# Performance work log

Measured on AMD Instinct MI355X. Metric: run time of the kernel, lower is better.

The kernel has to match this reference:

```python
import jax, jax.numpy as jnp
import numpy as np

HIDDEN = 2304
N_HEADS = 8
N_KV = 4
HEAD_DIM = 256
WINDOW = 1024
SOFTCAP = 50.0
EPS = 1e-6
SCALING = HEAD_DIM ** -0.5  # (head_dim * query_pre_attn_scalar=1.0) ** -0.5


def _rotate_half(x):
    d = x.shape[-1] // 2
    return jnp.concatenate([-x[..., d:], x[..., :d]], axis=-1)


def setup_inputs() -> dict:
    key = jax.random.key(0)
    ks = jax.random.split(key, 8)
    B, S = 2, 2048
    hidden_states = jax.random.normal(ks[0], (B, S, HIDDEN), dtype=jnp.float32)
    # RoPE tables, theta=10000
    inv_freq = 1.0 / (10000.0 ** (jnp.arange(0, HEAD_DIM, 2, dtype=jnp.float32) / HEAD_DIM))
    pos = jnp.arange(S, dtype=jnp.float32)
    freqs = pos[:, None] * inv_freq[None, :]              # [S, D/2]
    emb = jnp.concatenate([freqs, freqs], axis=-1)        # [S, D]
    cos = jnp.broadcast_to(jnp.cos(emb)[None], (B, S, HEAD_DIM)).astype(jnp.float32)
    sin = jnp.broadcast_to(jnp.sin(emb)[None], (B, S, HEAD_DIM)).astype(jnp.float32)
    std = 0.02
    rms_weight = jax.random.normal(ks[1], (HIDDEN,), dtype=jnp.float32) * std
    Wq = jax.random.normal(ks[2], (N_HEADS * HEAD_DIM, HIDDEN), dtype=jnp.float32) * std
    Wk = jax.random.normal(ks[3], (N_KV * HEAD_DIM, HIDDEN), dtype=jnp.float32) * std
    Wv = jax.random.normal(ks[4], (N_KV * HEAD_DIM, HIDDEN), dtype=jnp.float32) * std
    Wo = jax.random.normal(ks[5], (HIDDEN, N_HEADS * HEAD_DIM), dtype=jnp.float32) * std
    return {"hidden_states": hidden_states, "cos": cos, "sin": sin,
            "rms_weight": rms_weight, "Wq": Wq, "Wk": Wk, "Wv": Wv, "Wo": Wo}


def reference(hidden_states, cos, sin, rms_weight, Wq, Wk, Wv, Wo):
    B, S, H = hidden_states.shape
    # Gemma2 RMSNorm: x * rsqrt(mean(x^2)+eps) * (1 + w), computed in fp32
    xf = hidden_states.astype(jnp.float32)
    norm = xf * jax.lax.rsqrt(jnp.mean(xf * xf, axis=-1, keepdims=True) + EPS)
    x = (norm * (1.0 + rms_weight)).astype(hidden_states.dtype)

    q = jnp.einsum('bsh,dh->bsd', x, Wq).reshape(B, S, N_HEADS, HEAD_DIM).transpose(0, 2, 1, 3)
    k = jnp.einsum('bsh,dh->bsd', x, Wk).reshape(B, S, N_KV, HEAD_DIM).transpose(0, 2, 1, 3)
    v = jnp.einsum('bsh,dh->bsd', x, Wv).reshape(B, S, N_KV, HEAD_DIM).transpose(0, 2, 1, 3)

    c = cos[:, None, :, :]  # [B,1,S,D]
    s = sin[:, None, :, :]
    q = q * c + _rotate_half(q) * s
    k = k * c + _rotate_half(k) * s

    groups = N_HEADS // N_KV
    k = jnp.repeat(k, groups, axis=1)  # [B,Hq,S,D]
    v = jnp.repeat(v, groups, axis=1)

    scores = jnp.einsum('bhqd,bhkd->bhqk', q, k) * SCALING
    scores = SOFTCAP * jnp.tanh(scores / SOFTCAP)

    i = jnp.arange(S)[:, None]
    j = jnp.arange(S)[None, :]
    allowed = (j <= i) & ((i - j) < WINDOW)  # causal + sliding window
    scores = jnp.where(allowed[None, None], scores, jnp.float32(-1e30))

    w = jax.nn.softmax(scores.astype(jnp.float32), axis=-1).astype(q.dtype)
    attn = jnp.einsum('bhqk,bhkd->bhqd', w, v)
    attn = attn.transpose(0, 2, 1, 3).reshape(B, S, N_HEADS * HEAD_DIM)
    out = jnp.einsum('bsd,hd->bsh', attn, Wo)
    return hidden_states + out
```

## Files before the change

### kernel.cpp

```cpp
#include <hip/hip_runtime.h>
#include <cstdint>

typedef __bf16 bf16;
typedef __bf16 bf16x8 __attribute__((ext_vector_type(8)));
typedef __bf16 bf16x4 __attribute__((ext_vector_type(4)));
typedef float  f32x4  __attribute__((ext_vector_type(4)));

#define HIDDEN 2304
#define NQ 2048
#define NKV 1024
#define SEQ 2048

typedef __attribute__((address_space(1))) void gv_t;
typedef __attribute__((address_space(3))) void lv_t;
__device__ __forceinline__ void gld16(const void* g, void* l) {
  __builtin_amdgcn_global_load_lds((gv_t*)g, (lv_t*)l, 16, 0, 0);
}

#define BAR()    asm volatile("s_barrier" ::: "memory")
#define LGKM(n)  asm volatile("s_waitcnt lgkmcnt(" #n ")" ::: "memory")
#define VM6()    asm volatile("s_waitcnt vmcnt(6)" ::: "memory")
#define VM2()    asm volatile("s_waitcnt vmcnt(2)" ::: "memory")
#define VM0()    asm volatile("s_waitcnt vmcnt(0)" ::: "memory")
#define SCHED0() __builtin_amdgcn_sched_barrier(0)

__global__ __launch_bounds__(256) void rmsnorm_kernel(const float* __restrict__ x,
                                                      const float* __restrict__ w,
                                                      bf16* __restrict__ xb) {
  const int row = blockIdx.x, t = threadIdx.x;
  const float* xr = x + (size_t)row * HIDDEN;
  float v[9]; float ss = 0.f;
#pragma unroll
  for (int i = 0; i < 9; ++i) { v[i] = xr[t + i * 256]; ss += v[i] * v[i]; }
#pragma unroll
  for (int o = 32; o; o >>= 1) ss += __shfl_xor(ss, o, 64);
  __shared__ float wss[4];
  if ((t & 63) == 0) wss[t >> 6] = ss;
  __syncthreads();
  ss = wss[0] + wss[1] + wss[2] + wss[3];
  const float rs = rsqrtf(ss * (1.0f / HIDDEN) + 1e-6f);
  bf16* xo = xb + (size_t)row * HIDDEN;
#pragma unroll
  for (int i = 0; i < 9; ++i) xo[t + i * 256] = (bf16)(v[i] * rs * (1.0f + w[t + i * 256]));
}

#define NW0 (2048 * 2304)
#define NW1 (1024 * 2304)
#define NW3 (2304 * 2048)
__global__ __launch_bounds__(256) void cvt4_kernel(const float* __restrict__ s0, const float* __restrict__ s1,
                                                   const float* __restrict__ s2, const float* __restrict__ s3,
                                                   bf16* __restrict__ d0, bf16* __restrict__ d1,
                                                   bf16* __restrict__ d2, bf16* __restrict__ d3) {
  int i = (blockIdx.x * 256 + threadIdx.x) * 4;
  const float* s; bf16* dst; size_t oidx;
  if (i < NW0) {
    s = s0; const int r = i / 2304, c = i % 2304, d = r & 255;
    const int col = (((d >> 4) & 7) << 5) | ((d >> 7) << 4) | (d & 15);
    oidx = (size_t)((r & ~255) | col) * 2304 + c; dst = d0;
  } else if (i < NW0 + NW1) {
    i -= NW0;
    s = s1; const int r = i / 2304, c = i % 2304, d = r & 255;
    const int col = (((d >> 4) & 7) << 5) | ((d >> 7) << 4) | (d & 15);
    oidx = (size_t)((r & ~255) | col) * 2304 + c; dst = d1;
  } else if (i < NW0 + 2 * NW1) {
    i -= NW0 + NW1; s = s2; oidx = i; dst = d2;
  } else {
    i -= NW0 + 2 * NW1; s = s3; oidx = i; dst = d3;
  }
  const float4 f = *(const float4*)(s + i);
  bf16x4 o; o.x = (bf16)f.x; o.y = (bf16)f.y; o.z = (bf16)f.z; o.w = (bf16)f.w;
  *(bf16x4*)(dst + oidx) = o;
}

__device__ __forceinline__ void stage_half(const char* gbase, int stride, char* ldshalf, int tid) {
  const int c2 = ((tid & 7) * 16) ^ (((tid >> 3) & 7) << 4);
#pragma unroll
  for (int q = 0; q < 2; ++q) {
    const int r = q * 64 + (tid >> 3);
    gld16(gbase + (size_t)r * stride + c2, ldshalf + q * 8192 + tid * 16);
  }
}

template<int MH, int NH, int KS>
__device__ __forceinline__ void mfma_burst(const bf16x8 (&af)[4][2], const bf16x8 (&bn)[2][2],
                                           f32x4 (&acc)[8][4]) {
  __builtin_amdgcn_s_setprio(1);
#pragma unroll
  for (int m = 0; m < 4; ++m)
#pragma unroll
    for (int n = 0; n < 2; ++n)
      acc[MH * 4 + m][NH * 2 + n] =
          __builtin_amdgcn_mfma_f32_16x16x32_bf16(af[m][KS], bn[n][KS], acc[MH * 4 + m][NH * 2 + n], 0, 0, 0);
  __builtin_amdgcn_s_setprio(0);
}

template<int NT, int NY, int MODE>
__global__ __launch_bounds__(512) void gemm8p(const bf16* __restrict__ A, const bf16* __restrict__ B,
                                              bf16* __restrict__ Cq, bf16* __restrict__ Ck,
                                              bf16* __restrict__ Cvt, float* __restrict__ fo,
                                              const float* __restrict__ resid, int Nd,
                                              const float* __restrict__ cosb,
                                              const float* __restrict__ sinb) {
  __shared__ char lds[131072];
  const int Ks = NT * 128;
  const char* Aby = (const char*)A;
  const char* Bby = (const char*)B;

  int wg = blockIdx.x;
  const int chunk = (int)gridDim.x >> 3;
  wg = (wg & 7) * chunk + (wg >> 3);
  const int by = wg % NY, bx = wg / NY;
  const int m0 = bx * 256, n0 = by * 256;

  const int tid = threadIdx.x, lane = tid & 63, wv = tid >> 6;
  const int wm = wv >> 2, wn = wv & 3;
  const int r16 = lane & 15, g = lane >> 4;
  const int xr = (r16 & 7) << 4;
  const int cb0 = (g * 16) ^ xr, cb1 = (64 + g * 16) ^ xr;
  const int rdA = wm * 16384 + r16 * 128;
  const int rdB = 32768 + (wn >> 1) * 16384 + (wn & 1) * 8192 + r16 * 128;

  const char* A0g = Aby + (size_t)m0 * Ks;
  const char* A1g = Aby + (size_t)(m0 + 128) * Ks;
  const char* B0g = Bby + (size_t)n0 * Ks;
  const char* B1g = Bby + (size_t)(n0 + 128) * Ks;

  f32x4 acc[8][4] = {};
  bf16x8 a0[4][2], a1[4][2], bb01[2][2], bb23[2][2];

  auto read_a0bb01 = [&](const char* buf) {
#pragma unroll
    for (int n = 0; n < 2; ++n) bb01[n][0] = *(const bf16x8*)(buf + rdB + n * 2048 + cb0);
#pragma unroll
    for (int n = 0; n < 2; ++n) bb01[n][1] = *(const bf16x8*)(buf + rdB + n * 2048 + cb1);
#pragma unroll
    for (int m = 0; m < 4; ++m) a0[m][0] = *(const bf16x8*)(buf + rdA + m * 2048 + cb0);
#pragma unroll
    for (int m = 0; m < 4; ++m) a0[m][1] = *(const bf16x8*)(buf + rdA + m * 2048 + cb1);
  };

  stage_half(A0g, Ks, lds + 0,     tid);
  stage_half(A1g, Ks, lds + 16384, tid);
  stage_half(B0g, Ks, lds + 32768, tid);
  stage_half(B1g, Ks, lds + 49152, tid);
  stage_half(B0g + 128, Ks, lds + 65536 + 32768, tid);
  stage_half(A0g + 128, Ks, lds + 65536 + 0,     tid);
  stage_half(A1g + 128, Ks, lds + 65536 + 16384, tid);
  VM6(); BAR();
  read_a0bb01(lds);

  for (int t = 0; t < NT; ++t) {
    const char* bufc = lds + (size_t)(t & 1) * 65536;
    char* bufn = lds + (size_t)((t + 1) & 1) * 65536;
    char* bufs = lds + (size_t)(t & 1) * 65536;
    LGKM(0);
#pragma unroll
    for (int n = 0; n < 2; ++n) bb23[n][0] = *(const bf16x8*)(bufc + rdB + (2 + n) * 2048 + cb0);
#pragma unroll
    for (int n = 0; n < 2; ++n) bb23[n][1] = *(const bf16x8*)(bufc + rdB + (2 + n) * 2048 + cb1);
#pragma unroll
    for (int m = 0; m < 4; ++m) a1[m][0] = *(const bf16x8*)(bufc + rdA + 8192 + m * 2048 + cb0);
#pragma unroll
    for (int m = 0; m < 4; ++m) a1[m][1] = *(const bf16x8*)(bufc + rdA + 8192 + m * 2048 + cb1);
    SCHED0();
    mfma_burst<0, 0, 0>(a0, bb01, acc);
    mfma_burst<0, 0, 1>(a0, bb01, acc);
    SCHED0(); BAR();
    LGKM(8);
    if (t + 1 < NT)
      stage_half(B1g + (size_t)(t + 1) * 128, Ks, bufn + 49152, tid);
    SCHED0();
    mfma_burst<0, 1, 0>(a0, bb23, acc);
    mfma_burst<0, 1, 1>(a0, bb23, acc);
    SCHED0(); BAR();
    LGKM(0);
    if (t + 2 < NT)
      stage_half(B0g + (size_t)(t + 2) * 128, Ks, bufs + 32768, tid);
    SCHED0();
    mfma_burst<1, 0, 0>(a1, bb01, acc);
    mfma_burst<1, 0, 1>(a1, bb01, acc);
    SCHED0(); BAR();
    if (t < NT - 2) { VM2(); } else if (t == NT - 2) { VM0(); }
    if (t + 2 < NT) {
      stage_half(A0g + (size_t)(t + 2) * 128, Ks, bufs + 0,     tid);
      stage_half(A1g + (size_t)(t + 2) * 128, Ks, bufs + 16384, tid);
    }
    SCHED0();
    mfma_burst<1, 1, 0>(a1, bb23, acc);
    mfma_burst<1, 1, 1>(a1, bb23, acc);
    SCHED0(); BAR();
    if (t + 1 < NT) read_a0bb01(bufn);
  }

  const int mrow = m0 + wm * 128 + g * 4;
  if constexpr (MODE == 0) {
    if (n0 < 3072) {
      const bool isQ = (n0 < 2048);
      bf16* Cb = isQ ? (Cq + (size_t)0 * 0 + n0) : (Ck + (n0 - 2048));
      const int ld = isQ ? 2048 : 1024;
#pragma unroll
      for (int i = 0; i < 8; ++i)
#pragma unroll
        for (int jp = 0; jp < 2; ++jp) {
          const int col = wn * 64 + jp * 32 + r16;
          const int de = (col & 15) | (((col >> 5) & 7) << 4);
#pragma unroll
          for (int e = 0; e < 4; ++e) {
            const int m = mrow + i * 16 + e;
            const float c  = cosb[(size_t)m * 256 + de];
            const float sn = sinb[(size_t)m * 256 + de];
            const float v0 = acc[i][jp * 2][e];
            const float v1 = acc[i][jp * 2 + 1][e];
            Cb[(size_t)m * ld + de]       = (bf16)(v0 * c - v1 * sn);
            Cb[(size_t)m * ld + de + 128] = (bf16)(v1 * c + v0 * sn);
          }
        }
    } else {
      const int ncol = n0 + wn * 64 + r16;
#pragma unroll
      for (int i = 0; i < 8; ++i)
#pragma unroll
        for (int j = 0; j < 4; ++j)
#pragma unroll
          for (int e = 0; e < 4; ++e) {
            const int m = mrow + i * 16 + e;
            const int n = ncol + j * 16;
            const int b2 = m >> 11, s = m & 2047;
            Cvt[((size_t)b2 * 1024 + (n - 3072)) * SEQ + s] = (bf16)acc[i][j][e];
          }
    }
  } else {
    const int ncol = n0 + wn * 64 + r16;
#pragma unroll
    for (int i = 0; i < 8; ++i)
#pragma unroll
      for (int j = 0; j < 4; ++j)
#pragma unroll
        for (int e = 0; e < 4; ++e) {
          const int m = mrow + i * 16 + e;
          const int n = ncol + j * 16;
          fo[(size_t)m * Nd + n] = acc[i][j][e] + resid[(size_t)m * Nd + n];
        }
  }
}

__device__ __forceinline__ void attn_load(const bf16* __restrict__ kgp, const bf16* __restrict__ vgp,
                                          int j0, int t, bf16x8* kr, bf16x8* vr) {
#pragma unroll
  for (int it = 0; it < 4; ++it) {
    const int flat = it * 2048 + t * 8;
    kr[it] = *(const bf16x8*)&kgp[(size_t)((flat >> 8) + j0) * NKV + (flat & 255)];
    vr[it] = *(const bf16x8*)&vgp[(size_t)(flat >> 5) * SEQ + j0 + (flat & 31)];
  }
}

__global__ __launch_bounds__(256) void attn_kernel(const bf16* __restrict__ q, const bf16* __restrict__ k,
                                                   const bf16* __restrict__ vt, bf16* __restrict__ ao) {
  __shared__ bf16 smem[21248];
  bf16* const qs  = smem;
  bf16* const ksl = smem;
  bf16* const vtl = smem + 8448;
  bf16* const pl  = smem + 18688;
  int qt = blockIdx.x;
  const int h = blockIdx.y, b = blockIdx.z;
  if (b) qt = 31 - qt;
  const int kvh = h >> 1;
  const int t = threadIdx.x, lane = t & 63, w = t >> 6;
  const int r16 = lane & 15, g = lane >> 4;
  const int i_base = qt * 64;

  {
    const bf16* qg = q + ((size_t)(b * SEQ + i_base)) * NQ + h * 256;
#pragma unroll
    for (int it = 0; it < 8; ++it) {
      const int flat = it * 2048 + t * 8;
      const int row = flat >> 8, dd = flat & 255;
      *(bf16x8*)&qs[row * 264 + dd] = *(const bf16x8*)&qg[(size_t)row * NQ + dd];
    }
  }
  __syncthreads();
  bf16x8 aq[8];
#pragma unroll
  for (int c = 0; c < 8; ++c) aq[c] = *(const bf16x8*)&qs[(w * 16 + r16) * 264 + c * 32 + g * 8];

  f32x4 oacc[16] = {};
  float lrun[4] = {0.f, 0.f, 0.f, 0.f};
  int jb = i_base - 1023; if (jb < 0) jb = 0; jb &= ~31;
  const int je = i_base + 63;
  const bf16* kg = k + (size_t)b * SEQ * NKV + kvh * 256;
  const bf16* vg = vt + ((size_t)b * NKV + kvh * 256) * SEQ;

  bf16x8 kr[4], vr[4];
  attn_load(kg, vg, jb, t, kr, vr);

  for (int j0 = jb; j0 <= je; j0 += 32) {
    __syncthreads();
#pragma unroll
    for (int it = 0; it < 4; ++it) {
      const int flat = it * 2048 + t * 8;
      *(bf16x8*)&ksl[(flat >> 8) * 264 + (flat & 255)] = kr[it];
      *(bf16x8*)&vtl[(flat >> 5) * 40 + (flat & 31)] = vr[it];
    }
    __syncthreads();
    const int jn = (j0 + 32 <= je) ? (j0 + 32) : j0;
    attn_load(kg, vg, jn, t, kr, vr);

    f32x4 sc0 = {}, sc1 = {};
#pragma unroll
    for (int c = 0; c < 8; ++c) {
      const bf16x8 b0 = *(const bf16x8*)&ksl[r16 * 264 + c * 32 + g * 8];
      const bf16x8 b1 = *(const bf16x8*)&ksl[(16 + r16) * 264 + c * 32 + g * 8];
      sc0 = __builtin_amdgcn_mfma_f32_16x16x32_bf16(aq[c], b0, sc0, 0, 0, 0);
      sc1 = __builtin_amdgcn_mfma_f32_16x16x32_bf16(aq[c], b1, sc1, 0, 0, 0);
    }
    const bool full = (j0 + 31 <= i_base) && (i_base + 63 - j0 < 1024);
#pragma unroll
    for (int e = 0; e < 4; ++e) {
      const float t0 = __expf(sc0[e] * 0.0025f);
      const float t1 = __expf(sc1[e] * 0.0025f);
      float p0 = __expf(-100.0f / (t0 + 1.0f));
      float p1 = __expf(-100.0f / (t1 + 1.0f));
      if (!full) {
        const int irow = i_base + w * 16 + g * 4 + e;
        const int jg0 = j0 + r16, jg1 = j0 + 16 + r16;
        if (jg0 > irow || irow - jg0 >= 1024) p0 = 0.f;
        if (jg1 > irow || irow - jg1 >= 1024) p1 = 0.f;
      }
      const bf16 b0 = (bf16)p0, b1 = (bf16)p1;
      lrun[e] += (float)b0 + (float)b1;
      pl[w * 640 + (g * 4 + e) * 40 + r16] = b0;
      pl[w * 640 + (g * 4 + e) * 40 + 16 + r16] = b1;
    }
    const bf16x8 pa = *(const bf16x8*)&pl[w * 640 + r16 * 40 + g * 8];
#pragma unroll
    for (int nf = 0; nf < 16; ++nf) {
      const bf16x8 vb = *(const bf16x8*)&vtl[(nf * 16 + r16) * 40 + g * 8];
      oacc[nf] = __builtin_amdgcn_mfma_f32_16x16x32_bf16(pa, vb, oacc[nf], 0, 0, 0);
    }
  }
  float inv[4];
#pragma unroll
  for (int e = 0; e < 4; ++e) {
#pragma unroll
    for (int o = 1; o < 16; o <<= 1) lrun[e] += __shfl_xor(lrun[e], o, 64);
    inv[e] = 1.0f / lrun[e];
  }
  bf16* aor = ao + ((size_t)(b * SEQ + i_base + w * 16)) * NQ + h * 256;
#pragma unroll
  for (int nf = 0; nf < 16; ++nf)
#pragma unroll
    for (int e = 0; e < 4; ++e)
      aor[(size_t)(g * 4 + e) * NQ + nf * 16 + r16] = (bf16)(oacc[nf][e] * inv[e]);
}

extern "C" void kernel_launch(void* const* d_in, const int* in_sizes, int n_in,
                              void* d_out, int out_size, void* d_ws, size_t ws_size,
                              hipStream_t stream) {
  const float* hs   = (const float*)d_in[0];
  const float* cosb = (const float*)d_in[1];
  const float* sinb = (const float*)d_in[2];
  const float* rw   = (const float*)d_in[3];
  const float* Wq   = (const float*)d_in[4];
  const float* Wk   = (const float*)d_in[5];
  const float* Wv   = (const float*)d_in[6];
  const float* Wo   = (const float*)d_in[7];
  float* out = (float*)d_out;
  char* ws = (char*)d_ws;

  bf16* xb   = (bf16*)(ws);
  bf16* wqkv = (bf16*)(ws + 18874368);
  bf16* wkb  = wqkv + (size_t)2048 * 2304;
  bf16* wvb  = wqkv + (size_t)3072 * 2304;
  bf16* wob  = (bf16*)(ws + 37748736);
  bf16* qg   = (bf16*)(ws + 47185920);
  bf16* kg   = (bf16*)(ws + 63963136);
  bf16* vtg  = (bf16*)(ws + 72351744);
  bf16* ag   = (bf16*)(ws + 80740352);

  rmsnorm_kernel<<<4096, 256, 0, stream>>>(hs, rw, xb);
  cvt4_kernel<<<(NW0 + 2 * NW1 + NW3) / 4 / 256, 256, 0, stream>>>(Wq, Wk, Wv, Wo, wqkv, wkb, wvb, wob);
  gemm8p<36, 16, 0><<<256, 512, 0, stream>>>(xb, wqkv, qg, kg, vtg, nullptr, nullptr, 4096, cosb, sinb);
  attn_kernel<<<dim3(32, 8, 2), 256, 0, stream>>>(qg, kg, vtg, ag);
  gemm8p<32, 9, 1><<<144, 512, 0, stream>>>(ag, wob, nullptr, nullptr, nullptr, out, hs, 2304, nullptr, nullptr);
}
```

Baseline: 230.9 us.

## Restructure attention kernel with async LDS staging, 64-key tiles, and 2x2 warp split

Rewrites the attention inner loop to stage K, V and Q directly from global memory into XOR-swizzled LDS via global_load_lds, and to prefetch the next K and V tiles while the current tile computes. The KV tile grows from 32 to 64 keys, and the four waves now split 2x2 over query rows and key/head-dim halves, with softmax denominators combined through LDS at the end. This aims to cut register round-trips, LDS bank conflicts and per-tile barrier overhead, at the cost of much more LDS per block (about 75 KB), which may reduce occupancy.

```diff
diff --git a/kernel.cpp b/kernel.cpp
--- a/kernel.cpp
+++ b/kernel.cpp
@@ -19,6 +19,7 @@
 
 #define BAR()    asm volatile("s_barrier" ::: "memory")
 #define LGKM(n)  asm volatile("s_waitcnt lgkmcnt(" #n ")" ::: "memory")
+#define VM8()    asm volatile("s_waitcnt vmcnt(8)" ::: "memory")
 #define VM6()    asm volatile("s_waitcnt vmcnt(6)" ::: "memory")
 #define VM2()    asm volatile("s_waitcnt vmcnt(2)" ::: "memory")
 #define VM0()    asm volatile("s_waitcnt vmcnt(0)" ::: "memory")
@@ -196,7 +197,7 @@
   if constexpr (MODE == 0) {
     if (n0 < 3072) {
       const bool isQ = (n0 < 2048);
-      bf16* Cb = isQ ? (Cq + (size_t)0 * 0 + n0) : (Ck + (n0 - 2048));
+      bf16* Cb = isQ ? (Cq + n0) : (Ck + (n0 - 2048));
       const int ld = isQ ? 2048 : 1024;
 #pragma unroll
       for (int i = 0; i < 8; ++i)
@@ -244,113 +245,151 @@
   }
 }
 
-__device__ __forceinline__ void attn_load(const bf16* __restrict__ kgp, const bf16* __restrict__ vgp,
-                                          int j0, int t, bf16x8* kr, bf16x8* vr) {
-#pragma unroll
-  for (int it = 0; it < 4; ++it) {
-    const int flat = it * 2048 + t * 8;
-    kr[it] = *(const bf16x8*)&kgp[(size_t)((flat >> 8) + j0) * NKV + (flat & 255)];
-    vr[it] = *(const bf16x8*)&vgp[(size_t)(flat >> 5) * SEQ + j0 + (flat & 31)];
+__device__ __forceinline__ void stage_k64(const char* kgb, int j0, char* ksl, int t) {
+#pragma unroll
+  for (int p = 0; p < 8; ++p) {
+    const int o = p * 4096 + t * 16;
+    const int row = o >> 9, cb = o & 511;
+    gld16(kgb + (size_t)(j0 + row) * 2048 + (cb ^ ((row & 7) << 4)), ksl + o);
+  }
+}
+__device__ __forceinline__ void stage_v64(const char* vgb, int j0, char* vtl, int t) {
+#pragma unroll
+  for (int p = 0; p < 8; ++p) {
+    const int o = p * 4096 + t * 16;
+    const int row = o >> 7, cb = o & 127;
+    gld16(vgb + (size_t)row * 4096 + j0 * 2 + (cb ^ ((row & 7) << 4)), vtl + o);
+  }
+}
+__device__ __forceinline__ void stage_q64(const char* qgb, char* qs, int t) {
+#pragma unroll
+  for (int p = 0; p < 8; ++p) {
+    const int o = p * 4096 + t * 16;
+    const int row = o >> 9, cb = o & 511;
+    gld16(qgb + (size_t)row * 4096 + (cb ^ ((row & 7) << 4)), qs + o);
   }
 }
 
 __global__ __launch_bounds__(256) void attn_kernel(const bf16* __restrict__ q, const bf16* __restrict__ k,
                                                    const bf16* __restrict__ vt, bf16* __restrict__ ao) {
-  __shared__ bf16 smem[21248];
-  bf16* const qs  = smem;
-  bf16* const ksl = smem;
-  bf16* const vtl = smem + 8448;
-  bf16* const pl  = smem + 18688;
+  __shared__ char smem[75264];
+  char* const ksl = smem;
+  char* const vtl = smem + 32768;
+  bf16* const pl  = (bf16*)(smem + 65536);
+  float* const lbuf = (float*)(smem + 74752);
   int qt = blockIdx.x;
   const int h = blockIdx.y, b = blockIdx.z;
   if (b) qt = 31 - qt;
   const int kvh = h >> 1;
   const int t = threadIdx.x, lane = t & 63, w = t >> 6;
+  const int wq = w >> 1, wd = w & 1;
   const int r16 = lane & 15, g = lane >> 4;
+  const int xr = (r16 & 7) << 4;
   const int i_base = qt * 64;
-
-  {
-    const bf16* qg = q + ((size_t)(b * SEQ + i_base)) * NQ + h * 256;
-#pragma unroll
-    for (int it = 0; it < 8; ++it) {
-      const int flat = it * 2048 + t * 8;
-      const int row = flat >> 8, dd = flat & 255;
-      *(bf16x8*)&qs[row * 264 + dd] = *(const bf16x8*)&qg[(size_t)row * NQ + dd];
+  const int R0 = i_base + wq * 32;
+
+  const char* qgb = (const char*)(q + ((size_t)(b * SEQ + i_base)) * NQ + h * 256);
+  const char* kgb = (const char*)(k + (size_t)b * SEQ * NKV + kvh * 256);
+  const char* vgb = (const char*)(vt + ((size_t)b * NKV + kvh * 256) * SEQ);
+
+  stage_q64(qgb, ksl, t);
+  VM0(); BAR();
+  bf16x8 aq[2][8];
+#pragma unroll
+  for (int rg = 0; rg < 2; ++rg)
+#pragma unroll
+    for (int c = 0; c < 8; ++c)
+      aq[rg][c] = *(const bf16x8*)(ksl + (wq * 32 + rg * 16 + r16) * 512 + ((c * 64 + g * 16) ^ xr));
+  LGKM(0); BAR();
+
+  int jb = i_base - 1023; if (jb < 0) jb = 0; jb &= ~63;
+  const int je = i_base + 63;
+  stage_k64(kgb, jb, ksl, t);
+  stage_v64(vgb, jb, vtl, t);
+
+  f32x4 oacc[2][8] = {};
+  float lrun[2][4] = {};
+
+  for (int j0 = jb; j0 <= je; j0 += 64) {
+    const bool haveNext = (j0 + 64 <= je);
+    VM8(); BAR();
+    f32x4 sc[2][2] = {};
+#pragma unroll
+    for (int c = 0; c < 8; ++c) {
+      const int cb = (c * 64 + g * 16) ^ xr;
+      const bf16x8 b0 = *(const bf16x8*)(ksl + (wd * 32 + r16) * 512 + cb);
+      const bf16x8 b1 = *(const bf16x8*)(ksl + (wd * 32 + 16 + r16) * 512 + cb);
+      sc[0][0] = __builtin_amdgcn_mfma_f32_16x16x32_bf16(aq[0][c], b0, sc[0][0], 0, 0, 0);
+      sc[0][1] = __builtin_amdgcn_mfma_f32_16x16x32_bf16(aq[0][c], b1, sc[0][1], 0, 0, 0);
+      sc[1][0] = __builtin_amdgcn_mfma_f32_16x16x32_bf16(aq[1][c], b0, sc[1][0], 0, 0, 0);
+      sc[1][1] = __builtin_amdgcn_mfma_f32_16x16x32_bf16(aq[1][c], b1, sc[1][1], 0, 0, 0);
     }
-  }
-  __syncthreads();
-  bf16x8 aq[8];
-#pragma unroll
-  for (int c = 0; c < 8; ++c) aq[c] = *(const bf16x8*)&qs[(w * 16 + r16) * 264 + c * 32 + g * 8];
-
-  f32x4 oacc[16] = {};
-  float lrun[4] = {0.f, 0.f, 0.f, 0.f};
-  int jb = i_base - 1023; if (jb < 0) jb = 0; jb &= ~31;
-  const int je = i_base + 63;
-  const bf16* kg = k + (size_t)b * SEQ * NKV + kvh * 256;
-  const bf16* vg = vt + ((size_t)b * NKV + kvh * 256) * SEQ;
-
-  bf16x8 kr[4], vr[4];
-  attn_load(kg, vg, jb, t, kr, vr);
-
-  for (int j0 = jb; j0 <= je; j0 += 32) {
-    __syncthreads();
-#pragma unroll
-    for (int it = 0; it < 4; ++it) {
-      const int flat = it * 2048 + t * 8;
-      *(bf16x8*)&ksl[(flat >> 8) * 264 + (flat & 255)] = kr[it];
-      *(bf16x8*)&vtl[(flat >> 5) * 40 + (flat & 31)] = vr[it];
+    LGKM(0); BAR();
+    if (haveNext) stage_k64(kgb, j0 + 64, ksl, t);
+    const int J0 = j0 + wd * 32;
+    const bool full = (J0 + 31 <= R0) && (R0 - J0 <= 992);
+#pragma unroll
+    for (int rg = 0; rg < 2; ++rg)
+#pragma unroll
+      for (int e = 0; e < 4; ++e) {
+        const float t0 = __expf(sc[rg][0][e] * 0.0025f);
+        const float t1 = __expf(sc[rg][1][e] * 0.0025f);
+        float p0 = __expf(-100.0f / (t0 + 1.0f));
+        float p1 = __expf(-100.0f / (t1 + 1.0f));
+        if (!full) {
+          const int irow = R0 + rg * 16 + g * 4 + e;
+          const int jg0 = J0 + r16, jg1 = J0 + 16 + r16;
+          if (jg0 > irow || irow - jg0 >= 1024) p0 = 0.f;
+          if (jg1 > irow || irow - jg1 >= 1024) p1 = 0.f;
+        }
+        const bf16 pb0 = (bf16)p0, pb1 = (bf16)p1;
+        lrun[rg][e] += (float)pb0 + (float)pb1;
+        const int prow = wq * 32 + rg * 16 + g * 4 + e;
+        pl[prow * 72 + wd * 32 + r16] = pb0;
+        pl[prow * 72 + wd * 32 + 16 + r16] = pb1;
+      }
+    LGKM(0);
+    if (haveNext) { VM8(); } else { VM0(); }
+    BAR();
+#pragma unroll
+    for (int ks = 0; ks < 2; ++ks) {
+      const bf16x8 pa0 = *(const bf16x8*)(pl + (wq * 32 + r16) * 72 + ks * 32 + g * 8);
+      const bf16x8 pa1 = *(const bf16x8*)(pl + (wq * 32 + 16 + r16) * 72 + ks * 32 + g * 8);
+#pragma unroll
+      for (int nf = 0; nf < 8; ++nf) {
+        const bf16x8 vb = *(const bf16x8*)(vtl + (wd * 128 + nf * 16 + r16) * 128 + ((ks * 64 + g * 16) ^ xr));
+        oacc[0][nf] = __builtin_amdgcn_mfma_f32_16x16x32_bf16(pa0, vb, oacc[0][nf], 0, 0, 0);
+        oacc[1][nf] = __builtin_amdgcn_mfma_f32_16x16x32_bf16(pa1, vb, oacc[1][nf], 0, 0, 0);
+      }
     }
-    __syncthreads();
-    const int jn = (j0 + 32 <= je) ? (j0 + 32) : j0;
-    attn_load(kg, vg, jn, t, kr, vr);
-
-    f32x4 sc0 = {}, sc1 = {};
-#pragma unroll
-    for (int c = 0; c < 8; ++c) {
-      const bf16x8 b0 = *(const bf16x8*)&ksl[r16 * 264 + c * 32 + g * 8];
-      const bf16x8 b1 = *(const bf16x8*)&ksl[(16 + r16) * 264 + c * 32 + g * 8];
-      sc0 = __builtin_amdgcn_mfma_f32_16x16x32_bf16(aq[c], b0, sc0, 0, 0, 0);
-      sc1 = __builtin_amdgcn_mfma_f32_16x16x32_bf16(aq[c], b1, sc1, 0, 0, 0);
+    LGKM(0); BAR();
+    if (haveNext) stage_v64(vgb, j0 + 64, vtl, t);
+  }
+
+#pragma unroll
+  for (int rg = 0; rg < 2; ++rg)
+#pragma unroll
+    for (int e = 0; e < 4; ++e) {
+#pragma unroll
+      for (int o = 1; o < 16; o <<= 1) lrun[rg][e] += __shfl_xor(lrun[rg][e], o, 64);
+      if (r16 == 0) lbuf[w * 32 + rg * 16 + g * 4 + e] = lrun[rg][e];
     }
-    const bool full = (j0 + 31 <= i_base) && (i_base + 63 - j0 < 1024);
-#pragma unroll
-    for (int e = 0; e < 4; ++e) {
-      const float t0 = __expf(sc0[e] * 0.0025f);
-      const float t1 = __expf(sc1[e] * 0.0025f);
-      float p0 = __expf(-100.0f / (t0 + 1.0f));
-      float p1 = __expf(-100.0f / (t1 + 1.0f));
-      if (!full) {
-        const int irow = i_base + w * 16 + g * 4 + e;
-        const int jg0 = j0 + r16, jg1 = j0 + 16 + r16;
-        if (jg0 > irow || irow - jg0 >= 1024) p0 = 0.f;
-        if (jg1 > irow || irow - jg1 >= 1024) p1 = 0.f;
-      }
-      const bf16 b0 = (bf16)p0, b1 = (bf16)p1;
-      lrun[e] += (float)b0 + (float)b1;
-      pl[w * 640 + (g * 4 + e) * 40 + r16] = b0;
-      pl[w * 640 + (g * 4 + e) * 40 + 16 + r16] = b1;
-    }
-    const bf16x8 pa = *(const bf16x8*)&pl[w * 640 + r16 * 40 + g * 8];
-#pragma unroll
-    for (int nf = 0; nf < 16; ++nf) {
-      const bf16x8 vb = *(const bf16x8*)&vtl[(nf * 16 + r16) * 40 + g * 8];
-      oacc[nf] = __builtin_amdgcn_mfma_f32_16x16x32_bf16(pa, vb, oacc[nf], 0, 0, 0);
-    }
-  }
-  float inv[4];
-#pragma unroll
-  for (int e = 0; e < 4; ++e) {
-#pragma unroll
-    for (int o = 1; o < 16; o <<= 1) lrun[e] += __shfl_xor(lrun[e], o, 64);
-    inv[e] = 1.0f / lrun[e];
-  }
-  bf16* aor = ao + ((size_t)(b * SEQ + i_base + w * 16)) * NQ + h * 256;
-#pragma unroll
-  for (int nf = 0; nf < 16; ++nf)
+  LGKM(0); BAR();
+  float inv[2][4];
+#pragma unroll
+  for (int rg = 0; rg < 2; ++rg)
 #pragma unroll
     for (int e = 0; e < 4; ++e)
-      aor[(size_t)(g * 4 + e) * NQ + nf * 16 + r16] = (bf16)(oacc[nf][e] * inv[e]);
+      inv[rg][e] = 1.0f / (lrun[rg][e] + lbuf[(w ^ 1) * 32 + rg * 16 + g * 4 + e]);
+
+  bf16* aor = ao + ((size_t)(b * SEQ + R0)) * NQ + h * 256 + wd * 128;
+#pragma unroll
+  for (int rg = 0; rg < 2; ++rg)
+#pragma unroll
+    for (int nf = 0; nf < 8; ++nf)
+#pragma unroll
+      for (int e = 0; e < 4; ++e)
+        aor[(size_t)(rg * 16 + g * 4 + e) * NQ + nf * 16 + r16] = (bf16)(oacc[rg][nf][e] * inv[rg][e]);
 }
 
 extern "C" void kernel_launch(void* const* d_in, const int* in_sizes, int n_in,
```

Result: slower. 250.3 us (+8.4%).
